# Optimization experiments

Hardware: AMD Instinct MI355X
Metric: run time of the kernel (lower is better)

Reference implementation:

```python
import jax, jax.numpy as jnp
import numpy as np

B, T, D = 2, 2048, 2048
H = 8
KEY_DIM, VAL_DIM = 1024, 2048   # expand_k=0.5, expand_v=1.0
HK, HV = KEY_DIM // H, VAL_DIM // H
LOW_RANK = 16
GATE_NORM = 16.0
CHUNK = 64
HIDDEN = (D * 4 * 2 // 3 + 63) // 64 * 64  # 5504, exactly as GLUFFN.__init__
EPS = 1e-6


def rmsnorm(x, w):
    return x * jax.lax.rsqrt(jnp.mean(x * x, axis=-1, keepdims=True) + EPS) * w


def setup_inputs() -> dict:
    key = jax.random.key(0)
    ks = jax.random.split(key, 12)
    w = lambda k, s: jax.random.normal(k, s, jnp.float32) * 0.02
    return {
        "x": jax.random.normal(ks[0], (B, T, D), jnp.float32),
        "norm1_w": jnp.ones((D,), jnp.float32),
        "wq": w(ks[1], (D, KEY_DIM)),
        "wk": w(ks[2], (D, KEY_DIM)),
        "wv": w(ks[3], (D, VAL_DIM)),
        "gk_w1": w(ks[4], (D, LOW_RANK)),
        "gk_w2": w(ks[5], (LOW_RANK, KEY_DIM)),
        "gk_b": jnp.zeros((KEY_DIM,), jnp.float32),
        "wg": w(ks[6], (D, VAL_DIM)),
        "gnorm_w": jnp.ones((HV,), jnp.float32),
        "wo": w(ks[7], (VAL_DIM, D)),
        "ffn_norm_w": jnp.ones((D,), jnp.float32),
        "w_gate": w(ks[8], (D, HIDDEN)),
        "w_up": w(ks[9], (D, HIDDEN)),
        "w_down": w(ks[10], (HIDDEN, D)),
    }


def _gla(h, wq, wk, wv, gk_w1, gk_w2, gk_b, wg, gnorm_w, wo):
    # Gated linear attention, chunk-parallel form (fla-style):
    #   S_t = diag(exp(g_t)) S_{t-1} + k_t^T v_t ;  o_t = q_t S_t
    Bb, Tt, _ = h.shape
    nc = Tt // CHUNK

    def split(t, hd):  # [B,T,H*hd] -> [nc,B,H,CHUNK,hd]
        t = t.reshape(Bb, nc, CHUNK, H, hd)
        return jnp.transpose(t, (1, 0, 3, 2, 4))

    q = split(h @ wq, HK) * (HK ** -0.5)
    k = split(h @ wk, HK)
    v = split(h @ wv, HV)
    # low-rank forget gate, log-sigmoid scaled by gate_logit_normalizer=16
    g = split(jax.nn.log_sigmoid(h @ gk_w1 @ gk_w2 + gk_b) / GATE_NORM, HK)

    mask = jnp.tril(jnp.ones((CHUNK, CHUNK), jnp.float32))

    def step(S, inp):
        qc, kc, vc, gc = inp                       # [B,H,C,*]
        b = jnp.cumsum(gc, axis=-2)                # cumulative log-decay within chunk
        qe = qc * jnp.exp(b)
        A = jnp.einsum('bhik,bhjk->bhij', qe, kc * jnp.exp(-b)) * mask
        o = jnp.einsum('bhck,bhkv->bhcv', qe, S) + jnp.einsum('bhij,bhjv->bhiv', A, vc)
        bl = b[:, :, -1:, :]                       # decay to end of chunk
        S = jnp.exp(bl[:, :, 0, :])[..., None] * S + \
            jnp.einsum('bhck,bhcv->bhkv', kc * jnp.exp(bl - b), vc)
        return S, o

    S0 = jnp.zeros((Bb, H, HK, HV), h.dtype)
    _, o = jax.lax.scan(step, S0, (q, k, v, g))    # o: [nc,B,H,C,HV]
    o = jnp.transpose(o, (1, 0, 3, 2, 4)).reshape(Bb, Tt, H, HV)

    gate = (h @ wg).reshape(Bb, Tt, H, HV)
    # per-head RMSNorm + swish output gate (FusedRMSNormSwishGate)
    o = rmsnorm(o, gnorm_w) * gate * jax.nn.sigmoid(gate)
    return o.reshape(Bb, Tt, VAL_DIM) @ wo


def reference(x, norm1_w, wq, wk, wv, gk_w1, gk_w2, gk_b, wg, gnorm_w, wo,
              ffn_norm_w, w_gate, w_up, w_down):
    h = rmsnorm(x, norm1_w)
    x = x + _gla(h, wq, wk, wv, gk_w1, gk_w2, gk_b, wg, gnorm_w, wo)
    h2 = rmsnorm(x, ffn_norm_w)
    ffn = (jax.nn.silu(h2 @ w_gate) * (h2 @ w_up)) @ w_down  # GLUFFN, dropout=eval
    return x + ffn
```

## Files before the change

kernel.cpp:

```cpp
#include <hip/hip_runtime.h>

typedef unsigned short u16;
typedef __attribute__((ext_vector_type(8))) short bh8;
typedef __attribute__((ext_vector_type(4))) float f4;

__device__ __forceinline__ float bf2f(u16 u) {
  union { unsigned int i; float f; } x; x.i = ((unsigned int)u) << 16; return x.f;
}
__device__ __forceinline__ u16 f2bf(float f) {
  union { float f; unsigned int i; } x; x.f = f;
  unsigned int r = x.i + 0x7fffu + ((x.i >> 16) & 1u);
  return (u16)(r >> 16);
}
__device__ __forceinline__ f4 mfma16(bh8 a, bh8 b, f4 c) {
  return __builtin_amdgcn_mfma_f32_16x16x32_bf16(a, b, c, 0, 0, 0);
}
__device__ __forceinline__ void gload16(const void* g, void* l) {
  __builtin_amdgcn_global_load_lds(
      (const __attribute__((address_space(1))) void*)g,
      (__attribute__((address_space(3))) void*)l, 16, 0, 0);
}

__device__ __forceinline__ bh8 rd8(const u16* arr, int row, int col, int rowbytes) {
  return *(const bh8*)((const char*)arr + row * rowbytes + ((col * 2) ^ ((row & 7) << 4)));
}

struct WTJobs {
  const float* src[8];
  u16* dst[8];
  int R[8], C[8], rmul[8], roff[8], ntx[8], base[8];
};

__global__ __launch_bounds__(256)
void wtrans_all(WTJobs jobs) {
  __shared__ float tile[32][33];
  int bid = blockIdx.x;
  int ji = 0;
#pragma unroll
  for (int k = 1; k < 8; ++k) ji += (bid >= jobs.base[k]);
  int rel = bid - jobs.base[ji];
  int ntx = jobs.ntx[ji];
  int bx = rel % ntx, by = rel / ntx;
  const float* src = jobs.src[ji];
  u16* dst = jobs.dst[ji];
  int R = jobs.R[ji], C = jobs.C[ji], rmul = jobs.rmul[ji], roff = jobs.roff[ji];

  int tx = threadIdx.x & 31, ty = threadIdx.x >> 5;
  int c0 = bx * 32, r0 = by * 32;
#pragma unroll
  for (int yy = 0; yy < 32; yy += 8)
    tile[ty + yy][tx] = src[(size_t)(r0 + ty + yy) * C + c0 + tx];
  __syncthreads();
#pragma unroll
  for (int yy = 0; yy < 32; yy += 8)
    dst[(size_t)((c0 + ty + yy) * rmul + roff) * R + r0 + tx] = f2bf(tile[tx][ty + yy]);
}

__global__ __launch_bounds__(256)
void rmsnorm_k(const float* __restrict__ x, const float* __restrict__ w,
               u16* __restrict__ out) {
  int row = blockIdx.x, t = threadIdx.x;
  const float* xr = x + (size_t)row * 2048;
  float4 a = ((const float4*)xr)[t * 2];
  float4 b = ((const float4*)xr)[t * 2 + 1];
  float ss = a.x*a.x + a.y*a.y + a.z*a.z + a.w*a.w
           + b.x*b.x + b.y*b.y + b.z*b.z + b.w*b.w;
#pragma unroll
  for (int s = 32; s > 0; s >>= 1) ss += __shfl_xor(ss, s, 64);
  __shared__ float red[4];
  if ((t & 63) == 0) red[t >> 6] = ss;
  __syncthreads();
  float rr = rsqrtf((red[0] + red[1] + red[2] + red[3]) * (1.0f / 2048.0f) + 1e-6f);
  float v[8] = {a.x, a.y, a.z, a.w, b.x, b.y, b.z, b.w};
  int c0 = t * 8;
  u16* orow = out + (size_t)row * 2048 + c0;
#pragma unroll
  for (int j = 0; j < 8; ++j) orow[j] = f2bf(v[j] * rr * w[c0 + j]);
}

template <int EPI, typename OutT>
__global__ __launch_bounds__(512, 2)
void gemm2(const u16* __restrict__ A, const u16* __restrict__ Bt,
           OutT* __restrict__ C, void* __restrict__ aux, float scale,
           int M, int N, int K, int gx) {
  constexpr int SB = 32768;
  __shared__ char lds[3 * SB];
  int t = threadIdx.x, lane = t & 63, w = t >> 6;
  int c_ = lane & 15, r_ = lane >> 4;
  int wm = w >> 2, wn = w & 3;

  int nwg = gridDim.x;
  int wg = (blockIdx.x & 7) * (nwg >> 3) + (blockIdx.x >> 3);
  int gy = nwg / gx;
  int bx = wg / gy, by = wg % gy;
  int m0 = by * 256, n0 = bx * 256;

  const char* baseA[2];
#pragma unroll
  for (int h = 0; h < 2; ++h) {
    int p = h * 512 + t;
    int cc = p ^ ((p >> 3) & 7);
    baseA[h] = (const char*)A + ((size_t)(m0 + (cc >> 2)) * K + (cc & 3) * 8) * 2;
  }
  const char* baseB[2];
#pragma unroll
  for (int h = 0; h < 2; ++h) {
    int p = h * 512 + t;
    int cc = p ^ ((p >> 3) & 7);
    baseB[h] = (const char*)Bt + ((size_t)(n0 + (cc >> 2)) * K + (cc & 3) * 8) * 2;
  }
  int offA[8], offB[4];
#pragma unroll
  for (int mb = 0; mb < 8; ++mb) {
    int cc = (wm * 128 + mb * 16 + c_) * 4 + r_;
    offA[mb] = (cc ^ ((cc >> 3) & 7)) * 16;
  }
#pragma unroll
  for (int nb = 0; nb < 4; ++nb) {
    int cc = (wn * 64 + nb * 16 + c_) * 4 + r_;
    offB[nb] = (cc ^ ((cc >> 3) & 7)) * 16 + 16384;
  }
  int ldsW = w * 1024;

  f4 z4 = {0.f, 0.f, 0.f, 0.f};
  f4 acc[8][4];
#pragma unroll
  for (int mb = 0; mb < 8; ++mb)
#pragma unroll
    for (int nb = 0; nb < 4; ++nb) acc[mb][nb] = z4;

  int NT = K >> 5;

#define STAGEA(S, ko)                                                       \
  {                                                                         \
    _Pragma("unroll") for (int h = 0; h < 2; ++h)                           \
        gload16(baseA[h] + (ko), lds + (S) * SB + h * 8192 + ldsW);         \
  }
#define STAGEB(S, ko)                                                       \
  {                                                                         \
    _Pragma("unroll") for (int h = 0; h < 2; ++h)                           \
        gload16(baseB[h] + (ko), lds + (S) * SB + 16384 + h * 8192 + ldsW); \
  }
#define KTILE(S)                                                            \
  {                                                                         \
    int kts = kt + 2; if (kts >= NT) kts -= NT;                             \
    constexpr int S2 = ((S) + 2) % 3;                                       \
    bh8 fb[4], fa[4];                                                       \
    _Pragma("unroll") for (int nb = 0; nb < 4; ++nb)                        \
        fb[nb] = *(const bh8*)(lds + (S) * SB + offB[nb]);                  \
    _Pragma("unroll") for (int mb = 0; mb < 4; ++mb)                        \
        fa[mb] = *(const bh8*)(lds + (S) * SB + offA[mb]);                  \
    STAGEA(S2, kts << 6);                                                   \
    asm volatile("s_waitcnt lgkmcnt(0)" ::: "memory");                      \
    __builtin_amdgcn_sched_barrier(0);                                      \
    bh8 fa2[4];                                                             \
    _Pragma("unroll") for (int mb = 0; mb < 4; ++mb)                        \
        fa2[mb] = *(const bh8*)(lds + (S) * SB + offA[4 + mb]);             \
    STAGEB(S2, kts << 6);                                                   \
    __builtin_amdgcn_sched_barrier(0);                                      \
    __builtin_amdgcn_s_setprio(1);                                          \
    _Pragma("unroll") for (int mb = 0; mb < 4; ++mb)                        \
        _Pragma("unroll") for (int nb = 0; nb < 4; ++nb)                    \
            acc[mb][nb] = mfma16(fa[mb], fb[nb], acc[mb][nb]);              \
    __builtin_amdgcn_s_setprio(0);                                          \
    asm volatile("s_waitcnt lgkmcnt(0)" ::: "memory");                      \
    __builtin_amdgcn_sched_barrier(0);                                      \
    __builtin_amdgcn_s_setprio(1);                                          \
    _Pragma("unroll") for (int mb = 0; mb < 4; ++mb)                        \
        _Pragma("unroll") for (int nb = 0; nb < 4; ++nb)                    \
            acc[4 + mb][nb] = mfma16(fa2[mb], fb[nb], acc[4 + mb][nb]);     \
    __builtin_amdgcn_s_setprio(0);                                          \
    __builtin_amdgcn_sched_barrier(0);                                      \
    asm volatile("s_waitcnt vmcnt(4)" ::: "memory");                        \
    __builtin_amdgcn_s_barrier();                                           \
    asm volatile("" ::: "memory");                                          \
  }

  STAGEA(0, 0); STAGEB(0, 0);
  STAGEA(1, 64); STAGEB(1, 64);
  asm volatile("s_waitcnt vmcnt(4)" ::: "memory");
  __builtin_amdgcn_s_barrier();
  asm volatile("" ::: "memory");

  int kt = 0;
  while (true) {
    KTILE(0); if (++kt == NT) break;
    KTILE(1); if (++kt == NT) break;
    KTILE(2); if (++kt == NT) break;
  }
  asm volatile("s_waitcnt vmcnt(0)" ::: "memory");
#undef KTILE
#undef STAGEA
#undef STAGEB

  int rowBase = m0 + wm * 128;
#pragma unroll
  for (int mb = 0; mb < 8; ++mb) {
#pragma unroll
    for (int rr = 0; rr < 4; ++rr) {
      int row = rowBase + mb * 16 + r_ * 4 + rr;
#pragma unroll
      for (int nb = 0; nb < 4; ++nb) {
        int col = n0 + wn * 64 + nb * 16 + c_;
        float val = acc[mb][nb][rr];
        if (EPI == 4) {
          if (col < 2048) {
            int bb = row >> 11, t2 = row & 2047;
            int pan = ((bb << 5) + (t2 >> 6)) * 8 + (col >> 8);
            int ii = t2 & 63, vv = col & 255;
            *(u16*)((char*)C + (size_t)pan * 32768 + vv * 128 + ((ii * 2) ^ ((vv & 7) << 4)))
                = f2bf(val);
          } else {
            ((u16*)aux)[(size_t)row * 2048 + col - 2048] = f2bf(val);
          }
        } else if (EPI == 6) {
          float other = __shfl_xor(val, 1, 64);
          if (lane & 1) {
            float gv = other;
            ((u16*)C)[(size_t)row * 5504 + (col >> 1)] = f2bf(val * (gv / (1.f + expf(-gv))));
          }
        }
      }
    }
  }
}

template <int EPI, typename OutT>
__global__ __launch_bounds__(512, 2)
void gemm3(const u16* __restrict__ A, const u16* __restrict__ Bt,
           OutT* __restrict__ C, void* __restrict__ aux, float scale,
           int M, int N, int K, int gx) {
  constexpr int SB = 49152;
  __shared__ char lds[2 * SB];
  int t = threadIdx.x, lane = t & 63, w = t >> 6;
  int c_ = lane & 15, r_ = lane >> 4;
  int wm = w >> 1, wn = w & 1;

  int nwg = gridDim.x;
  int wg = (blockIdx.x & 7) * (nwg >> 3) + (blockIdx.x >> 3);
  int gy = nwg / gx;
  int bx = wg / gy, by = wg % gy;
  int m0 = by * 256, n0 = bx * 128;

  int trow = t >> 3;
  int kchunk = (t & 7) ^ (trow & 7);
  const char* baseA[4];
#pragma unroll
  for (int l = 0; l < 4; ++l)
    baseA[l] = (const char*)A + ((size_t)(m0 + l * 64 + trow) * K + kchunk * 8) * 2;
  const char* baseB[2];
#pragma unroll
  for (int l = 0; l < 2; ++l)
    baseB[l] = (const char*)Bt + ((size_t)(n0 + l * 64 + trow) * K + kchunk * 8) * 2;

  int offA[4][2], offB[4][2];
#pragma unroll
  for (int mb = 0; mb < 4; ++mb) {
    int row = wm * 64 + mb * 16 + c_;
#pragma unroll
    for (int ks = 0; ks < 2; ++ks)
      offA[mb][ks] = row * 128 + (((ks * 4 + r_) ^ (row & 7)) << 4);
  }
#pragma unroll
  for (int nb = 0; nb < 4; ++nb) {
    int n = wn * 64 + nb * 16 + c_;
#pragma unroll
    for (int ks = 0; ks < 2; ++ks)
      offB[nb][ks] = 32768 + n * 128 + (((ks * 4 + r_) ^ (n & 7)) << 4);
  }
  int ldsW = w * 1024;

  f4 z4 = {0.f, 0.f, 0.f, 0.f};
  f4 acc[4][4];
#pragma unroll
  for (int mb = 0; mb < 4; ++mb)
#pragma unroll
    for (int nb = 0; nb < 4; ++nb) acc[mb][nb] = z4;

  int NT = K >> 6;

#define STAGE(S, ko)                                                        \
  {                                                                         \
    _Pragma("unroll") for (int l = 0; l < 4; ++l)                           \
        gload16(baseA[l] + (ko), lds + (S) * SB + l * 8192 + ldsW);         \
    _Pragma("unroll") for (int l = 0; l < 2; ++l)                           \
        gload16(baseB[l] + (ko), lds + (S) * SB + 32768 + l * 8192 + ldsW); \
  }
#define KT64(S)                                                             \
  {                                                                         \
    int kts = kt + 1; if (kts >= NT) kts -= NT;                             \
    STAGE((S) ^ 1, kts << 7);                                               \
    _Pragma("unroll")                                                       \
    for (int ks = 0; ks < 2; ++ks) {                                        \
      bh8 fb[4], fa[4];                                                     \
      _Pragma("unroll") for (int nb = 0; nb < 4; ++nb)                      \
          fb[nb] = *(const bh8*)(lds + (S) * SB + offB[nb][ks]);            \
      _Pragma("unroll") for (int mb = 0; mb < 4; ++mb)                      \
          fa[mb] = *(const bh8*)(lds + (S) * SB + offA[mb][ks]);            \
      asm volatile("s_waitcnt lgkmcnt(0)" ::: "memory");                    \
      __builtin_amdgcn_sched_barrier(0);                                    \
      __builtin_amdgcn_s_setprio(1);                                        \
      _Pragma("unroll") for (int mb = 0; mb < 4; ++mb)                      \
          _Pragma("unroll") for (int nb = 0; nb < 4; ++nb)                  \
              acc[mb][nb] = mfma16(fa[mb], fb[nb], acc[mb][nb]);            \
      __builtin_amdgcn_s_setprio(0);                                        \
      __builtin_amdgcn_sched_barrier(0);                                    \
    }                                                                       \
    asm volatile("s_waitcnt vmcnt(0)" ::: "memory");                        \
    __builtin_amdgcn_s_barrier();                                           \
    asm volatile("" ::: "memory");                                          \
  }

  STAGE(0, 0);
  asm volatile("s_waitcnt vmcnt(0)" ::: "memory");
  __builtin_amdgcn_s_barrier();
  asm volatile("" ::: "memory");

  int kt = 0;
  while (true) {
    KT64(0); if (++kt == NT) break;
    KT64(1); if (++kt == NT) break;
  }
#undef KT64
#undef STAGE

  int rowBase = m0 + wm * 64;
#pragma unroll
  for (int mb = 0; mb < 4; ++mb) {
#pragma unroll
    for (int rr = 0; rr < 4; ++rr) {
      int row = rowBase + mb * 16 + r_ * 4 + rr;
#pragma unroll
      for (int nb = 0; nb < 4; ++nb) {
        int col = n0 + wn * 64 + nb * 16 + c_;
        float val = acc[mb][nb][rr];
        if (EPI == 1) {
          ((float*)C)[(size_t)row * N + col] = val + ((const float*)aux)[(size_t)row * N + col];
        } else if (EPI == 5) {
          if (col < 1024) ((u16*)C)[(size_t)row * 1024 + col] = f2bf(val * scale);
          else ((u16*)aux)[(size_t)row * 1024 + col - 1024] = f2bf(val);
        }
      }
    }
  }
}

__global__ __launch_bounds__(256)
void lowrank_k(const u16* __restrict__ h, const float* __restrict__ w1,
               const float* __restrict__ w2, const float* __restrict__ bias,
               float* __restrict__ g) {
  int row = blockIdx.x, t = threadIdx.x, lane = t & 63, wave = t >> 6;
  const u16* hr = h + (size_t)row * 2048;
  bh8 hv = *(const bh8*)&hr[t * 8];
  float p[16];
#pragma unroll
  for (int j = 0; j < 16; ++j) p[j] = 0.f;
#pragma unroll
  for (int kk = 0; kk < 8; ++kk) {
    float f = bf2f((u16)hv[kk]);
    const float* wrow = w1 + (size_t)(t * 8 + kk) * 16;
#pragma unroll
    for (int j = 0; j < 16; ++j) p[j] += f * wrow[j];
  }
#pragma unroll
  for (int j = 0; j < 16; ++j)
#pragma unroll
    for (int s = 32; s > 0; s >>= 1) p[j] += __shfl_xor(p[j], s, 64);
  __shared__ float gl[4][16];
  if (lane == 0) {
#pragma unroll
    for (int j = 0; j < 16; ++j) gl[wave][j] = p[j];
  }
  __syncthreads();
  float glow[16];
#pragma unroll
  for (int j = 0; j < 16; ++j) glow[j] = gl[0][j] + gl[1][j] + gl[2][j] + gl[3][j];
  float* grow = g + (size_t)row * 1024;
#pragma unroll
  for (int nn = 0; nn < 4; ++nn) {
    int n = nn * 256 + t;
    float z = bias[n];
#pragma unroll
    for (int j = 0; j < 16; ++j) z += glow[j] * w2[j * 1024 + n];
    float ls = fminf(z, 0.f) - log1pf(expf(-fabsf(z)));
    grow[n] = ls * (1.0f / 16.0f);
  }
}

__global__ __launch_bounds__(128)
void gprep_k(u16* __restrict__ q, u16* __restrict__ k, const float* __restrict__ g,
             u16* __restrict__ keT, float* __restrict__ ebl) {
  int bid = blockIdx.x;
  int h = bid & 7, bc = bid >> 3;
  int b = bc >> 5, c = bc & 31;
  int ch = threadIdx.x;
  size_t base = ((size_t)(b * 2048 + c * 64)) * 1024 + h * 128 + ch;
  char* keTp = (char*)keT + (size_t)bid * 16384 + ch * 128;
  int sw = (ch & 7) << 4;
  float bacc = 0.f;
  for (int i8 = 0; i8 < 8; ++i8) {
    u16 kp[8];
#pragma unroll
    for (int e = 0; e < 8; ++e) {
      size_t off = base + (size_t)(i8 * 8 + e) * 1024;
      bacc += g[off];
      float eb = __expf(bacc);
      float reb = __builtin_amdgcn_rcpf(eb);
      float qv = bf2f(q[off]), kv = bf2f(k[off]);
      q[off] = f2bf(qv * eb);
      u16 kev = f2bf(kv * reb);
      k[off] = kev;
      kp[e] = kev;
    }
    *(bh8*)(keTp + ((i8 * 16) ^ sw)) = *(const bh8*)kp;
  }
  ebl[(size_t)bid * 128 + ch] = __expf(bacc);
}

__global__ __launch_bounds__(256)
void gla_scan(const u16* __restrict__ qg, const u16* __restrict__ kg,
              const u16* __restrict__ keTg, const u16* __restrict__ vTg,
              const float* __restrict__ eblg, float* __restrict__ outp) {
  __shared__ u16 qeL[64 * 128];
  __shared__ u16 keL[64 * 128];
  __shared__ u16 kTL[128 * 64];
  __shared__ u16 vTL[64 * 64];
  __shared__ u16 AL[64 * 64];
  __shared__ u16 SbL[64 * 128];
  __shared__ float SfL[64][133];

  int t = threadIdx.x, lane = t & 63, w = t >> 6;
  int vb = blockIdx.x & 3, bh = blockIdx.x >> 2;
  int b = bh >> 3, h = bh & 7;
  int c_ = lane & 15, r_ = lane >> 4;
  f4 z4 = {0.f, 0.f, 0.f, 0.f};

  for (int i = t; i < 64 * 128; i += 256) SbL[i] = 0;
  for (int i = t; i < 64 * 133; i += 256) ((float*)SfL)[i] = 0.f;

  const char* qbase = (const char*)qg + (size_t)b * 2048 * 2048 + h * 256;
  const char* kbase = (const char*)kg + (size_t)b * 2048 * 2048 + h * 256;
  int rowoff = (t >> 4) * 2048 + (t & 15) * 16;
  int4 pq[4], pk[4], pkt[4], pvt[2];

#define LOADCH(cc)                                                              \
  {                                                                             \
    const char* qc = qbase + (size_t)(cc) * 64 * 2048;                          \
    const char* kc = kbase + (size_t)(cc) * 64 * 2048;                          \
    int panel_ = ((b * 32 + (cc)) * 8 + h);                                     \
    const char* ktc = (const char*)keTg + (size_t)panel_ * 16384;               \
    const char* vtc = (const char*)vTg + (size_t)panel_ * 32768 + vb * 8192;    \
    _Pragma("unroll")                                                           \
    for (int j = 0; j < 4; ++j) {                                               \
      pq[j] = *(const int4*)(qc + j * 16 * 2048 + rowoff);                      \
      pk[j] = *(const int4*)(kc + j * 16 * 2048 + rowoff);                      \
      pkt[j] = *(const int4*)(ktc + j * 4096 + t * 16);                         \
    }                                                                           \
    _Pragma("unroll")                                                           \
    for (int j = 0; j < 2; ++j) pvt[j] = *(const int4*)(vtc + j * 4096 + t * 16); \
  }

  LOADCH(0);
  for (int c = 0; c < 32; ++c) {
#pragma unroll
    for (int j = 0; j < 4; ++j) {
      int L = j * 4096 + t * 16;
      int d = (L & ~255) | ((L & 255) ^ (((L >> 8) & 7) << 4));
      *(int4*)((char*)qeL + d) = pq[j];
      *(int4*)((char*)keL + d) = pk[j];
      *(int4*)((char*)kTL + L) = pkt[j];
    }
#pragma unroll
    for (int j = 0; j < 2; ++j) *(int4*)((char*)vTL + j * 4096 + t * 16) = pvt[j];
    if (c < 31) LOADCH(c + 1);
    int panel = ((b * 32 + c) * 8 + h);
    float eblr[2][4];
#pragma unroll
    for (int kt = 0; kt < 2; ++kt)
#pragma unroll
      for (int r = 0; r < 4; ++r)
        eblr[kt][r] = eblg[(size_t)panel * 128 + w * 32 + kt * 16 + r_ * 4 + r];
    __syncthreads();

    f4 accA[4] = {z4, z4, z4, z4};
    f4 accS[2][4] = {{z4, z4, z4, z4}, {z4, z4, z4, z4}};
#pragma unroll
    for (int ks = 0; ks < 4; ++ks) {
      bh8 a = rd8(qeL, w * 16 + c_, ks * 32 + r_ * 8, 256);
#pragma unroll
      for (int n = 0; n < 4; ++n)
        accA[n] = mfma16(a, rd8(keL, n * 16 + c_, ks * 32 + r_ * 8, 256), accA[n]);
    }
#pragma unroll
    for (int ks = 0; ks < 2; ++ks) {
      bh8 bf_[4];
#pragma unroll
      for (int n = 0; n < 4; ++n) bf_[n] = rd8(vTL, n * 16 + c_, ks * 32 + r_ * 8, 128);
#pragma unroll
      for (int kt = 0; kt < 2; ++kt) {
        bh8 a = rd8(kTL, w * 32 + kt * 16 + c_, ks * 32 + r_ * 8, 128);
#pragma unroll
        for (int n = 0; n < 4; ++n) accS[kt][n] = mfma16(a, bf_[n], accS[kt][n]);
      }
    }
#pragma unroll
    for (int n = 0; n < 4; ++n)
#pragma unroll
      for (int r = 0; r < 4; ++r) {
        int i = w * 16 + r_ * 4 + r, j = n * 16 + c_;
        *(u16*)((char*)AL + i * 128 + ((j * 2) ^ ((i & 7) << 4))) =
            (j <= i) ? f2bf(accA[n][r]) : (u16)0;
      }
    __syncthreads();

    f4 acco[4] = {z4, z4, z4, z4};
#pragma unroll
    for (int ks = 0; ks < 4; ++ks) {
      bh8 a = rd8(qeL, w * 16 + c_, ks * 32 + r_ * 8, 256);
#pragma unroll
      for (int n = 0; n < 4; ++n)
        acco[n] = mfma16(a, rd8(SbL, n * 16 + c_, ks * 32 + r_ * 8, 256), acco[n]);
    }
#pragma unroll
    for (int ks = 0; ks < 2; ++ks) {
      bh8 a = rd8(AL, w * 16 + c_, ks * 32 + r_ * 8, 128);
#pragma unroll
      for (int n = 0; n < 4; ++n)
        acco[n] = mfma16(a, rd8(vTL, n * 16 + c_, ks * 32 + r_ * 8, 128), acco[n]);
    }
    {
      size_t obase = (size_t)(b * 2048 + c * 64 + w * 16 + r_ * 4) * 2048 + h * 256 + vb * 64;
#pragma unroll
      for (int n = 0; n < 4; ++n)
#pragma unroll
        for (int r = 0; r < 4; ++r)
          outp[obase + (size_t)r * 2048 + n * 16 + c_] = acco[n][r];
    }
    __syncthreads();

#pragma unroll
    for (int kt = 0; kt < 2; ++kt)
#pragma unroll
      for (int n = 0; n < 4; ++n)
#pragma unroll
        for (int r = 0; r < 4; ++r) {
          int kk = w * 32 + kt * 16 + r_ * 4 + r;
          int vcol = n * 16 + c_;
          float nv = eblr[kt][r] * (SfL[vcol][kk] + accS[kt][n][r]);
          SfL[vcol][kk] = nv;
          *(u16*)((char*)SbL + vcol * 256 + ((kk * 2) ^ ((vcol & 7) << 4))) = f2bf(nv);
        }
    __syncthreads();
  }
#undef LOADCH
}

__global__ __launch_bounds__(256)
void ogate_k(const float* __restrict__ o, const u16* __restrict__ gate,
             const float* __restrict__ gw, u16* __restrict__ og) {
  int tok = blockIdx.x, t = threadIdx.x;
  int head = t >> 5, l32 = t & 31, v0 = l32 * 8;
  size_t base = (size_t)tok * 2048 + head * 256 + v0;
  float4 a = *(const float4*)&o[base];
  float4 b = *(const float4*)&o[base + 4];
  float ov[8] = {a.x, a.y, a.z, a.w, b.x, b.y, b.z, b.w};
  float ss = 0.f;
#pragma unroll
  for (int j = 0; j < 8; ++j) ss += ov[j] * ov[j];
#pragma unroll
  for (int s = 16; s > 0; s >>= 1) ss += __shfl_xor(ss, s, 32);
  float rr = rsqrtf(ss * (1.0f / 256.0f) + 1e-6f);
#pragma unroll
  for (int j = 0; j < 8; ++j) {
    float gv = bf2f(gate[base + j]);
    float val = ov[j] * rr * gw[v0 + j];
    og[base + j] = f2bf(val * gv / (1.f + expf(-gv)));
  }
}

extern "C" void kernel_launch(void* const* d_in, const int* in_sizes, int n_in,
                              void* d_out, int out_size, void* d_ws, size_t ws_size,
                              hipStream_t stream) {
  (void)in_sizes; (void)n_in; (void)out_size; (void)ws_size;
  const float* x = (const float*)d_in[0];
  const float* n1w = (const float*)d_in[1];
  const float* wq = (const float*)d_in[2];
  const float* wk = (const float*)d_in[3];
  const float* wv = (const float*)d_in[4];
  const float* gw1 = (const float*)d_in[5];
  const float* gw2 = (const float*)d_in[6];
  const float* gb = (const float*)d_in[7];
  const float* wg = (const float*)d_in[8];
  const float* gnw = (const float*)d_in[9];
  const float* wo = (const float*)d_in[10];
  const float* fnw = (const float*)d_in[11];
  const float* wgate = (const float*)d_in[12];
  const float* wup = (const float*)d_in[13];
  const float* wdown = (const float*)d_in[14];
  float* out = (float*)d_out;

  char* ws = (char*)d_ws;
  size_t off = 0;
  auto alloc = [&](size_t bytes) { size_t p = off; off += (bytes + 255) & ~(size_t)255; return p; };
  u16* wqT = (u16*)(ws + alloc(2ull * 1024 * 2048));
  u16* wkT = (u16*)(ws + alloc(2ull * 1024 * 2048));
  u16* wvT = (u16*)(ws + alloc(2ull * 2048 * 2048));
  u16* wgT = (u16*)(ws + alloc(2ull * 2048 * 2048));
  u16* woT = (u16*)(ws + alloc(2ull * 2048 * 2048));
  u16* btGU = (u16*)(ws + alloc(2ull * 11008 * 2048));
  u16* wdT = (u16*)(ws + alloc(2ull * 2048 * 5504));
  u16* h_bf = (u16*)(ws + alloc(2ull * 4096 * 2048));
  u16* q_bf = (u16*)(ws + alloc(2ull * 4096 * 1024));
  u16* k_bf = (u16*)(ws + alloc(2ull * 4096 * 1024));
  u16* vT_g = (u16*)(ws + alloc(2ull * 4096 * 2048));
  u16* gate_bf = (u16*)(ws + alloc(2ull * 4096 * 2048));
  float* g_f = (float*)(ws + alloc(4ull * 4096 * 1024));
  float* o_f = (float*)(ws + alloc(4ull * 4096 * 2048));
  u16* mid = (u16*)(ws + alloc(2ull * 4096 * 5504));
  float* ebl_g = (float*)(ws + alloc(4ull * 512 * 128));
  u16* keT_g = h_bf;
  u16* og = h_bf;
  u16* h2 = q_bf;
  float* x2 = o_f;

  dim3 blk(256);
  dim3 blk2(512);

  WTJobs jobs;
  const float* srcs[8] = {wq, wk, wv, wg, wo, wgate, wup, wdown};
  u16* dsts[8] = {wqT, wkT, wvT, wgT, woT, btGU, btGU, wdT};
  int Rs[8] = {2048, 2048, 2048, 2048, 2048, 2048, 2048, 5504};
  int Cs[8] = {1024, 1024, 2048, 2048, 2048, 5504, 5504, 2048};
  int rmuls[8] = {1, 1, 1, 1, 1, 2, 2, 1};
  int roffs[8] = {0, 0, 0, 0, 0, 0, 1, 0};
  int nb = 0;
  for (int j = 0; j < 8; ++j) {
    jobs.src[j] = srcs[j]; jobs.dst[j] = dsts[j];
    jobs.R[j] = Rs[j]; jobs.C[j] = Cs[j];
    jobs.rmul[j] = rmuls[j]; jobs.roff[j] = roffs[j];
    jobs.ntx[j] = Cs[j] / 32;
    jobs.base[j] = nb;
    nb += (Cs[j] / 32) * (Rs[j] / 32);
  }
  wtrans_all<<<nb, blk, 0, stream>>>(jobs);

  rmsnorm_k<<<4096, blk, 0, stream>>>(x, n1w, h_bf);

  gemm3<5, u16><<<256, blk2, 0, stream>>>(h_bf, wqT, q_bf, k_bf, 0.08838834764831845f,
                                          4096, 2048, 2048, 16);
  gemm2<4, u16><<<256, blk2, 0, stream>>>(h_bf, wvT, vT_g, gate_bf, 1.f,
                                          4096, 4096, 2048, 16);
  lowrank_k<<<4096, blk, 0, stream>>>(h_bf, gw1, gw2, gb, g_f);

  gprep_k<<<512, dim3(128), 0, stream>>>(q_bf, k_bf, g_f, keT_g, ebl_g);

  gla_scan<<<64, blk, 0, stream>>>(q_bf, k_bf, keT_g, vT_g, ebl_g, o_f);

  ogate_k<<<4096, blk, 0, stream>>>(o_f, gate_bf, gnw, og);

  gemm3<1, float><<<256, blk2, 0, stream>>>(og, woT, x2, (void*)x, 1.f,
                                            4096, 2048, 2048, 16);

  rmsnorm_k<<<4096, blk, 0, stream>>>(x2, fnw, h2);

  gemm2<6, u16><<<688, blk2, 0, stream>>>(h2, btGU, mid, nullptr, 1.f,
                                          4096, 11008, 2048, 43);
  gemm3<1, float><<<256, blk2, 0, stream>>>(mid, wdT, out, x2, 1.f,
                                            4096, 2048, 5504, 16);
}
```

Before: 930.7 us.

## Replace triple-buffered K32 GEMM pipeline with double-buffered K64 tiles

The gemm2 kernel becomes gemm4. It now stages 64-wide K tiles into two 64KB LDS buffers, replacing the previous three 32KB buffers with 32-wide K. Each iteration issues the next tile's loads, then runs two K32 sub-steps of MFMAs using XOR-swizzled offsets, then waits on vmcnt(0) before the barrier. The goal is to halve the number of barriers and loop iterations and to issue larger load batches. In exchange the kernel uses 128KB of LDS per block, which likely limits occupancy to one block per CU, and prefetch depth drops from two tiles to one.

```diff
diff --git a/kernel.cpp b/kernel.cpp
--- a/kernel.cpp
+++ b/kernel.cpp
@@ -80,11 +80,11 @@
 
 template <int EPI, typename OutT>
 __global__ __launch_bounds__(512, 2)
-void gemm2(const u16* __restrict__ A, const u16* __restrict__ Bt,
+void gemm4(const u16* __restrict__ A, const u16* __restrict__ Bt,
            OutT* __restrict__ C, void* __restrict__ aux, float scale,
            int M, int N, int K, int gx) {
-  constexpr int SB = 32768;
-  __shared__ char lds[3 * SB];
+  constexpr int SB = 65536;
+  __shared__ char lds[2 * SB];
   int t = threadIdx.x, lane = t & 63, w = t >> 6;
   int c_ = lane & 15, r_ = lane >> 4;
   int wm = w >> 2, wn = w & 3;
@@ -95,30 +95,22 @@
   int bx = wg / gy, by = wg % gy;
   int m0 = by * 256, n0 = bx * 256;
 
-  const char* baseA[2];
-#pragma unroll
-  for (int h = 0; h < 2; ++h) {
-    int p = h * 512 + t;
-    int cc = p ^ ((p >> 3) & 7);
-    baseA[h] = (const char*)A + ((size_t)(m0 + (cc >> 2)) * K + (cc & 3) * 8) * 2;
-  }
-  const char* baseB[2];
-#pragma unroll
-  for (int h = 0; h < 2; ++h) {
-    int p = h * 512 + t;
-    int cc = p ^ ((p >> 3) & 7);
-    baseB[h] = (const char*)Bt + ((size_t)(n0 + (cc >> 2)) * K + (cc & 3) * 8) * 2;
-  }
+  int trow = t >> 3;
+  int kchunk = (t & 7) ^ (trow & 7);
+  const char* baseA = (const char*)A + ((size_t)(m0 + trow) * K + kchunk * 8) * 2;
+  const char* baseB = (const char*)Bt + ((size_t)(n0 + trow) * K + kchunk * 8) * 2;
+  size_t rowStride = (size_t)64 * K * 2;
+
   int offA[8], offB[4];
 #pragma unroll
   for (int mb = 0; mb < 8; ++mb) {
-    int cc = (wm * 128 + mb * 16 + c_) * 4 + r_;
-    offA[mb] = (cc ^ ((cc >> 3) & 7)) * 16;
+    int row = wm * 128 + mb * 16 + c_;
+    offA[mb] = row * 128 + ((r_ ^ (row & 7)) << 4);
   }
 #pragma unroll
   for (int nb = 0; nb < 4; ++nb) {
-    int cc = (wn * 64 + nb * 16 + c_) * 4 + r_;
-    offB[nb] = (cc ^ ((cc >> 3) & 7)) * 16 + 16384;
+    int n = wn * 64 + nb * 16 + c_;
+    offB[nb] = 32768 + n * 128 + ((r_ ^ (n & 7)) << 4);
   }
   int ldsW = w * 1024;
 
@@ -129,69 +121,54 @@
 #pragma unroll
     for (int nb = 0; nb < 4; ++nb) acc[mb][nb] = z4;
 
-  int NT = K >> 5;
-
-#define STAGEA(S, ko)                                                       \
-  {                                                                         \
-    _Pragma("unroll") for (int h = 0; h < 2; ++h)                           \
-        gload16(baseA[h] + (ko), lds + (S) * SB + h * 8192 + ldsW);         \
-  }
-#define STAGEB(S, ko)                                                       \
-  {                                                                         \
-    _Pragma("unroll") for (int h = 0; h < 2; ++h)                           \
-        gload16(baseB[h] + (ko), lds + (S) * SB + 16384 + h * 8192 + ldsW); \
-  }
-#define KTILE(S)                                                            \
-  {                                                                         \
-    int kts = kt + 2; if (kts >= NT) kts -= NT;                             \
-    constexpr int S2 = ((S) + 2) % 3;                                       \
-    bh8 fb[4], fa[4];                                                       \
-    _Pragma("unroll") for (int nb = 0; nb < 4; ++nb)                        \
-        fb[nb] = *(const bh8*)(lds + (S) * SB + offB[nb]);                  \
-    _Pragma("unroll") for (int mb = 0; mb < 4; ++mb)                        \
-        fa[mb] = *(const bh8*)(lds + (S) * SB + offA[mb]);                  \
-    STAGEA(S2, kts << 6);                                                   \
-    asm volatile("s_waitcnt lgkmcnt(0)" ::: "memory");                      \
-    __builtin_amdgcn_sched_barrier(0);                                      \
-    bh8 fa2[4];                                                             \
-    _Pragma("unroll") for (int mb = 0; mb < 4; ++mb)                        \
-        fa2[mb] = *(const bh8*)(lds + (S) * SB + offA[4 + mb]);             \
-    STAGEB(S2, kts << 6);                                                   \
-    __builtin_amdgcn_sched_barrier(0);                                      \
-    __builtin_amdgcn_s_setprio(1);                                          \
-    _Pragma("unroll") for (int mb = 0; mb < 4; ++mb)                        \
-        _Pragma("unroll") for (int nb = 0; nb < 4; ++nb)                    \
-            acc[mb][nb] = mfma16(fa[mb], fb[nb], acc[mb][nb]);              \
-    __builtin_amdgcn_s_setprio(0);                                          \
-    asm volatile("s_waitcnt lgkmcnt(0)" ::: "memory");                      \
-    __builtin_amdgcn_sched_barrier(0);                                      \
-    __builtin_amdgcn_s_setprio(1);                                          \
-    _Pragma("unroll") for (int mb = 0; mb < 4; ++mb)                        \
-        _Pragma("unroll") for (int nb = 0; nb < 4; ++nb)                    \
-            acc[4 + mb][nb] = mfma16(fa2[mb], fb[nb], acc[4 + mb][nb]);     \
-    __builtin_amdgcn_s_setprio(0);                                          \
-    __builtin_amdgcn_sched_barrier(0);                                      \
-    asm volatile("s_waitcnt vmcnt(4)" ::: "memory");                        \
-    __builtin_amdgcn_s_barrier();                                           \
-    asm volatile("" ::: "memory");                                          \
-  }
-
-  STAGEA(0, 0); STAGEB(0, 0);
-  STAGEA(1, 64); STAGEB(1, 64);
-  asm volatile("s_waitcnt vmcnt(4)" ::: "memory");
+  int NT = K >> 6;
+
+#define STAGE(S, ko)                                                          \
+  {                                                                           \
+    _Pragma("unroll") for (int l = 0; l < 4; ++l)                             \
+        gload16(baseA + l * rowStride + (ko), lds + (S) * SB + l * 8192 + ldsW); \
+    _Pragma("unroll") for (int l = 0; l < 4; ++l)                             \
+        gload16(baseB + l * rowStride + (ko),                                 \
+                lds + (S) * SB + 32768 + l * 8192 + ldsW);                    \
+  }
+#define KT64(S)                                                               \
+  {                                                                           \
+    int kts = kt + 1; if (kts >= NT) kts -= NT;                               \
+    STAGE((S) ^ 1, kts << 7);                                                 \
+    _Pragma("unroll")                                                         \
+    for (int ks = 0; ks < 2; ++ks) {                                          \
+      const int kx = ks ? 64 : 0;                                             \
+      bh8 fb[4], fa[8];                                                       \
+      _Pragma("unroll") for (int nb = 0; nb < 4; ++nb)                        \
+          fb[nb] = *(const bh8*)(lds + (S) * SB + (offB[nb] ^ kx));           \
+      _Pragma("unroll") for (int mb = 0; mb < 8; ++mb)                        \
+          fa[mb] = *(const bh8*)(lds + (S) * SB + (offA[mb] ^ kx));           \
+      asm volatile("s_waitcnt lgkmcnt(0)" ::: "memory");                      \
+      __builtin_amdgcn_sched_barrier(0);                                      \
+      __builtin_amdgcn_s_setprio(1);                                          \
+      _Pragma("unroll") for (int mb = 0; mb < 8; ++mb)                        \
+          _Pragma("unroll") for (int nb = 0; nb < 4; ++nb)                    \
+              acc[mb][nb] = mfma16(fa[mb], fb[nb], acc[mb][nb]);              \
+      __builtin_amdgcn_s_setprio(0);                                          \
+      __builtin_amdgcn_sched_barrier(0);                                      \
+    }                                                                         \
+    asm volatile("s_waitcnt vmcnt(0)" ::: "memory");                          \
+    __builtin_amdgcn_s_barrier();                                             \
+    asm volatile("" ::: "memory");                                            \
+  }
+
+  STAGE(0, 0);
+  asm volatile("s_waitcnt vmcnt(0)" ::: "memory");
   __builtin_amdgcn_s_barrier();
   asm volatile("" ::: "memory");
 
   int kt = 0;
   while (true) {
-    KTILE(0); if (++kt == NT) break;
-    KTILE(1); if (++kt == NT) break;
-    KTILE(2); if (++kt == NT) break;
-  }
-  asm volatile("s_waitcnt vmcnt(0)" ::: "memory");
-#undef KTILE
-#undef STAGEA
-#undef STAGEB
+    KT64(0); if (++kt == NT) break;
+    KT64(1); if (++kt == NT) break;
+  }
+#undef KT64
+#undef STAGE
 
   int rowBase = m0 + wm * 128;
 #pragma unroll
@@ -648,7 +625,7 @@
 
   gemm3<5, u16><<<256, blk2, 0, stream>>>(h_bf, wqT, q_bf, k_bf, 0.08838834764831845f,
                                           4096, 2048, 2048, 16);
-  gemm2<4, u16><<<256, blk2, 0, stream>>>(h_bf, wvT, vT_g, gate_bf, 1.f,
+  gemm4<4, u16><<<256, blk2, 0, stream>>>(h_bf, wvT, vT_g, gate_bf, 1.f,
                                           4096, 4096, 2048, 16);
   lowrank_k<<<4096, blk, 0, stream>>>(h_bf, gw1, gw2, gb, g_f);
 
@@ -663,7 +640,7 @@
 
   rmsnorm_k<<<4096, blk, 0, stream>>>(x2, fnw, h2);
 
-  gemm2<6, u16><<<688, blk2, 0, stream>>>(h2, btGU, mid, nullptr, 1.f,
+  gemm4<6, u16><<<688, blk2, 0, stream>>>(h2, btGU, mid, nullptr, 1.f,
                                           4096, 11008, 2048, 43);
   gemm3<1, float><<<256, blk2, 0, stream>>>(mid, wdT, out, x2, 1.f,
                                             4096, 2048, 5504, 16);
```

Measured after the change: 1.951 ms. 110% more time.
